# Performance work log

Hardware: AMD Instinct MI355X
Metric: run time of the kernel (lower is better)

The kernel has to match this reference:

```python
import jax, jax.numpy as jnp
import numpy as np


def setup_inputs() -> dict:
    key = jax.random.key(0)
    x = jax.random.uniform(key, (16, 1024, 512), dtype=jnp.float32)
    return {"x": x, "n_bits": 10}


def reference(x, n_bits):
    # Successive-approximation binary encoding: bit i fires if the residual
    # signal exceeds 2^-(i+1); residual is reduced by that threshold when it fires.
    v = jnp.clip(x, 0.0, 1.0)  # [B, T, C]
    bits = []
    decision = 0.5
    for _ in range(n_bits):
        s = (v >= decision).astype(x.dtype)
        bits.append(s)
        v = v - s * decision
        decision = decision * 0.5
    # stack along new bit axis -> [B, T, n_bits, C]
    return jnp.stack(bits, axis=2)
```

## Files before the change

### kernel.cpp

```cpp
#include <hip/hip_runtime.h>


#define C_DIM 512

typedef float f32x4 __attribute__((ext_vector_type(4)));

__global__ __launch_bounds__(256) void binenc_kernel(const float* __restrict__ x,
                                                     const int* __restrict__ n_bits_p,
                                                     float* __restrict__ out,
                                                     int n_vec) {
    const int n_bits = *n_bits_p;
    const float scale = (float)(1u << n_bits);
    const int   maxq  = (1 << n_bits) - 1;

    const int vid = blockIdx.x * blockDim.x + threadIdx.x;
    if (vid >= n_vec) return;

    const f32x4 xin = __builtin_nontemporal_load(reinterpret_cast<const f32x4*>(x) + vid);

    const int fidx = vid << 2;
    const int row  = fidx >> 9;
    const int c    = fidx & (C_DIM - 1);

    int q[4];
#pragma unroll
    for (int j = 0; j < 4; ++j) {
        float v = fminf(fmaxf(xin[j], 0.0f), 1.0f);
        int qi = (int)(v * scale);
        q[j] = qi > maxq ? maxq : qi;
    }

    float* outbase = out + row * n_bits * C_DIM + c;
    for (int i = 0; i < n_bits; ++i) {
        const int sh = n_bits - 1 - i;
        f32x4 s;
#pragma unroll
        for (int j = 0; j < 4; ++j)
            s[j] = (float)((q[j] >> sh) & 1);
        __builtin_nontemporal_store(s, reinterpret_cast<f32x4*>(outbase + i * C_DIM));
    }
}

extern "C" void kernel_launch(void* const* d_in, const int* in_sizes, int n_in,
                              void* d_out, int out_size, void* d_ws, size_t ws_size,
                              hipStream_t stream) {
    const float* x        = (const float*)d_in[0];
    const int*   n_bits_p = (const int*)d_in[1];
    float*       out      = (float*)d_out;

    const int n_elems = in_sizes[0];
    const int n_vec   = n_elems >> 2;
    const int block   = 256;
    const int grid    = (n_vec + block - 1) / block;

    binenc_kernel<<<grid, block, 0, stream>>>(x, n_bits_p, out, n_vec);
}
```

Before: 77.70 us.

## Map one block per row, split bit planes across thread halves

Each block now handles one (B,T) row. Each thread redundantly loads one float4 of input, and the two 128-thread halves write alternating bit planes, so each store instruction covers a contiguous 256-vector span of the output row. Nontemporal load/store hints are dropped in favour of plain accesses. The input is read twice (once per half), and the write loop becomes shorter per thread, which changes memory coalescing and parallelism on a write-bound kernel.

```diff
diff --git a/kernel.cpp b/kernel.cpp
--- a/kernel.cpp
+++ b/kernel.cpp
@@ -2,42 +2,41 @@
 
 
 #define C_DIM 512
+#define C4    128
 
 typedef float f32x4 __attribute__((ext_vector_type(4)));
 
 __global__ __launch_bounds__(256) void binenc_kernel(const float* __restrict__ x,
                                                      const int* __restrict__ n_bits_p,
-                                                     float* __restrict__ out,
-                                                     int n_vec) {
+                                                     float* __restrict__ out) {
     const int n_bits = *n_bits_p;
     const float scale = (float)(1u << n_bits);
     const int   maxq  = (1 << n_bits) - 1;
 
-    const int vid = blockIdx.x * blockDim.x + threadIdx.x;
-    if (vid >= n_vec) return;
+    const int row  = blockIdx.x;
+    const int tid  = threadIdx.x;
+    const int c4   = tid & (C4 - 1);
+    const int bit0 = tid >> 7;
 
-    const f32x4 xin = __builtin_nontemporal_load(reinterpret_cast<const f32x4*>(x) + vid);
-
-    const int fidx = vid << 2;
-    const int row  = fidx >> 9;
-    const int c    = fidx & (C_DIM - 1);
+    const f32x4 xv = reinterpret_cast<const f32x4*>(x)[row * C4 + c4];
 
     int q[4];
 #pragma unroll
     for (int j = 0; j < 4; ++j) {
-        float v = fminf(fmaxf(xin[j], 0.0f), 1.0f);
-        int qi = (int)(v * scale);
+        float v  = fminf(fmaxf(xv[j], 0.0f), 1.0f);
+        int   qi = (int)(v * scale);
         q[j] = qi > maxq ? maxq : qi;
     }
 
-    float* outbase = out + row * n_bits * C_DIM + c;
-    for (int i = 0; i < n_bits; ++i) {
-        const int sh = n_bits - 1 - i;
+    f32x4* rowbase = reinterpret_cast<f32x4*>(out) + (size_t)row * n_bits * C4;
+#pragma unroll 5
+    for (int k = 0; 2 * k + bit0 < n_bits; ++k) {
+        const int sh = n_bits - 1 - (2 * k + bit0);
         f32x4 s;
 #pragma unroll
         for (int j = 0; j < 4; ++j)
             s[j] = (float)((q[j] >> sh) & 1);
-        __builtin_nontemporal_store(s, reinterpret_cast<f32x4*>(outbase + i * C_DIM));
+        rowbase[k * 256 + tid] = s;
     }
 }
 
@@ -48,10 +47,8 @@
     const int*   n_bits_p = (const int*)d_in[1];
     float*       out      = (float*)d_out;
 
-    const int n_elems = in_sizes[0];
-    const int n_vec   = n_elems >> 2;
-    const int block   = 256;
-    const int grid    = (n_vec + block - 1) / block;
+    const int n_rows = in_sizes[0] / C_DIM;
+    const int block  = 256;
 
-    binenc_kernel<<<grid, block, 0, stream>>>(x, n_bits_p, out, n_vec);
+    binenc_kernel<<<n_rows, block, 0, stream>>>(x, n_bits_p, out);
 }
```

New measurement: 73.23 us. -5.7%, faster.
